# Optimization experiments

Hardware: AMD Instinct MI355X
Metric: run time of the kernel (lower is better)

## Reference

```python
import jax, jax.numpy as jnp
import numpy as np

H, B, T, C = 1024, 256, 256, 10

def setup_inputs() -> dict:
    key = jax.random.key(0)
    ks = jax.random.split(key, 10)
    def xav(k, shape):
        fan_in, fan_out = shape[1], shape[0]
        lim = jnp.sqrt(6.0 / (fan_in + fan_out))
        return jax.random.uniform(k, shape, jnp.float32, -lim, lim)
    return {
        "x": jax.random.normal(ks[0], (B, T), jnp.float32),
        "W_gx": xav(ks[1], (H, 1)), "W_gh": xav(ks[2], (H, H)),
        "W_ix": xav(ks[3], (H, 1)), "W_ih": xav(ks[4], (H, H)),
        "W_fx": xav(ks[5], (H, 1)), "W_fh": xav(ks[6], (H, H)),
        "W_ox": xav(ks[7], (H, 1)), "W_oh": xav(ks[8], (H, H)),
        "W_ph": xav(ks[9], (C, H)),
        "b_g": jnp.zeros((B,), jnp.float32), "b_i": jnp.zeros((B,), jnp.float32),
        "b_f": jnp.zeros((B,), jnp.float32), "b_o": jnp.zeros((B,), jnp.float32),
        "b_p": jnp.zeros((B,), jnp.float32),
    }

def reference(x, W_gx, W_gh, W_ix, W_ih, W_fx, W_fh, W_ox, W_oh, W_ph,
              b_g, b_i, b_f, b_o, b_p):
    batch = x.shape[0]
    hidden = W_gh.shape[0]
    xs = x.T  # [T, B]; per-step x_t is a [1, B] row (input_dim = 1)

    def step(carry, x_t):
        h, c = carry                       # [H, B] each
        xr = x_t[None, :]                  # [1, B]
        g = jnp.tanh(W_gx @ xr + W_gh @ h + b_g)          # [H, B] + [B] broadcasts per column
        i = jax.nn.sigmoid(W_ix @ xr + W_ih @ h + b_i)
        f = jax.nn.sigmoid(W_fx @ xr + W_fh @ h + b_f)
        o = jax.nn.sigmoid(W_ox @ xr + W_oh @ h + b_o)
        c_new = g * i + c * f
        h_new = jnp.tanh(c_new) * o
        return (h_new, c_new), None

    h0 = jnp.zeros((hidden, batch), x.dtype)
    c0 = jnp.zeros((hidden, batch), x.dtype)
    (h_T, _), _ = jax.lax.scan(step, (h0, c0), xs)
    p = W_ph @ h_T + b_p                   # [C, B]
    y = jax.nn.softmax(p, axis=1)          # faithful: softmax over dim=1 (batch axis)
    return y.T                             # [B, C]
```

## Files before the change

kernel.cpp:

```cpp
#include <hip/hip_runtime.h>
#include <hip/hip_bf16.h>


#define H 1024
#define B 256
#define T 256
#define NCLS 10

typedef __attribute__((ext_vector_type(8))) short short8;
typedef __attribute__((ext_vector_type(4))) float f32x4;

__device__ inline unsigned short bf16_bits(float f) {
    union { __hip_bfloat16 h; unsigned short u; } cv;
    cv.h = __float2bfloat16(f);
    return cv.u;
}


__global__ __launch_bounds__(512)
__attribute__((amdgpu_waves_per_eu(2, 2)))
void lstm_persist(
    const float* __restrict__ x,
    const float* __restrict__ Wgh, const float* __restrict__ Wih,
    const float* __restrict__ Wfh, const float* __restrict__ Woh,
    const float* __restrict__ Wgx, const float* __restrict__ Wix,
    const float* __restrict__ Wfx, const float* __restrict__ Wox,
    const float* __restrict__ bg, const float* __restrict__ bi,
    const float* __restrict__ bf_, const float* __restrict__ bo,
    char* __restrict__ frag,
    unsigned* __restrict__ flags,
    float* __restrict__ hfin)
{
    __shared__ __align__(16) char hstage[65536];
    __shared__ float zb[2][4][32][36];
    __shared__ float wxl[4][32];
    __shared__ float bsl[4][32];

    const int tid  = threadIdx.x;
    const int lane = tid & 63;
    const int wave = tid >> 6;
    const int gate = wave & 3;
    const int kh   = wave >> 2;
    const int bt = blockIdx.x & 7;
    const int jt = blockIdx.x >> 3;
    const int j0 = jt * 32;
    const int b0 = bt * 32;

    if (tid < 128) {
        int g = tid >> 5, r = tid & 31;
        const float* wx = (g == 0) ? Wgx : (g == 1) ? Wix : (g == 2) ? Wfx : Wox;
        const float* bb = (g == 0) ? bg  : (g == 1) ? bi  : (g == 2) ? bf_ : bo;
        wxl[g][r] = wx[j0 + r];
        bsl[g][r] = bb[b0 + r];
    }

    const float* Wh = (gate == 0) ? Wgh : (gate == 1) ? Wih : (gate == 2) ? Wfh : Woh;
    short8 awreg[2][16];
#pragma unroll
    for (int mt = 0; mt < 2; ++mt) {
        const float* wrow = Wh + (j0 + 16 * mt + (lane & 15)) * H
                          + kh * 512 + ((lane >> 4) * 8);
#pragma unroll
        for (int c = 0; c < 16; ++c) {
            const float4 f0 = *(const float4*)(wrow + c * 32);
            const float4 f1 = *(const float4*)(wrow + c * 32 + 4);
            short8 s;
            s[0] = (short)bf16_bits(f0.x); s[1] = (short)bf16_bits(f0.y);
            s[2] = (short)bf16_bits(f0.z); s[3] = (short)bf16_bits(f0.w);
            s[4] = (short)bf16_bits(f1.x); s[5] = (short)bf16_bits(f1.y);
            s[6] = (short)bf16_bits(f1.z); s[7] = (short)bf16_bits(f1.w);
            awreg[mt][c] = s;
        }
    }
#pragma unroll
    for (int mt = 0; mt < 2; ++mt)
#pragma unroll
        for (int c = 0; c < 16; ++c)
            __asm__ volatile("" : "+a"(awreg[mt][c]));

    float creg[2] = {0.f, 0.f};
    const int nn = tid & 31;
    const int aa = tid >> 5;

    unsigned* myflag = &flags[blockIdx.x * 32];
    unsigned* pollflag = &flags[(((unsigned)lane & 31) * 8 + bt) * 32];

    for (int t = 0; t < T; ++t) {
        const float xv = x[(b0 + nn) * T + t];

        if (wave == 0) {
            const unsigned target = (unsigned)t;
            while (true) {
                unsigned v = __hip_atomic_load(pollflag, __ATOMIC_RELAXED,
                                               __HIP_MEMORY_SCOPE_AGENT);
                if (__all((int)(v >= target))) break;
                __builtin_amdgcn_s_sleep(1);
            }
        }
        __syncthreads();

        {
            const char* gbase = frag + (t & 1) * 524288 + bt * 65536 + tid * 16;
            short8 v0, v1, v2, v3, v4, v5, v6, v7;
            __asm__ volatile(
                "global_load_dwordx4 %0, %8, off sc0 sc1\n\t"
                "global_load_dwordx4 %1, %9, off sc0 sc1\n\t"
                "global_load_dwordx4 %2, %10, off sc0 sc1\n\t"
                "global_load_dwordx4 %3, %11, off sc0 sc1\n\t"
                "global_load_dwordx4 %4, %12, off sc0 sc1\n\t"
                "global_load_dwordx4 %5, %13, off sc0 sc1\n\t"
                "global_load_dwordx4 %6, %14, off sc0 sc1\n\t"
                "global_load_dwordx4 %7, %15, off sc0 sc1\n\t"
                "s_waitcnt vmcnt(0)"
                : "=&v"(v0), "=&v"(v1), "=&v"(v2), "=&v"(v3),
                  "=&v"(v4), "=&v"(v5), "=&v"(v6), "=&v"(v7)
                : "v"(gbase),         "v"(gbase + 8192),
                  "v"(gbase + 16384), "v"(gbase + 24576),
                  "v"(gbase + 32768), "v"(gbase + 40960),
                  "v"(gbase + 49152), "v"(gbase + 57344)
                : "memory");
            short8* dd = (short8*)hstage;
            dd[tid +    0] = v0;  dd[tid +  512] = v1;
            dd[tid + 1024] = v2;  dd[tid + 1536] = v3;
            dd[tid + 2048] = v4;  dd[tid + 2560] = v5;
            dd[tid + 3072] = v6;  dd[tid + 3584] = v7;
        }
        __syncthreads();

        f32x4 a00 = {0.f,0.f,0.f,0.f}, a01 = a00, a10 = a00, a11 = a00;
#pragma unroll
        for (int c = 0; c < 16; ++c) {
            const int cg = kh * 16 + c;
            short8 bf0 = *(const short8*)(hstage + cg * 1024 + lane * 16);
            short8 bf1 = *(const short8*)(hstage + 32768 + cg * 1024 + lane * 16);
            a00 = __builtin_amdgcn_mfma_f32_16x16x32_bf16(awreg[0][c], bf0, a00, 0, 0, 0);
            a01 = __builtin_amdgcn_mfma_f32_16x16x32_bf16(awreg[0][c], bf1, a01, 0, 0, 0);
            a10 = __builtin_amdgcn_mfma_f32_16x16x32_bf16(awreg[1][c], bf0, a10, 0, 0, 0);
            a11 = __builtin_amdgcn_mfma_f32_16x16x32_bf16(awreg[1][c], bf1, a11, 0, 0, 0);
        }

        {
            const int cn = lane & 15;
            const int rb = (lane >> 4) * 4;
#pragma unroll
            for (int r = 0; r < 4; ++r) {
                zb[kh][gate][ 0 + rb + r][ 0 + cn] = a00[r];
                zb[kh][gate][ 0 + rb + r][16 + cn] = a01[r];
                zb[kh][gate][16 + rb + r][ 0 + cn] = a10[r];
                zb[kh][gate][16 + rb + r][16 + cn] = a11[r];
            }
        }
        __syncthreads();

        unsigned short hb[2];
#pragma unroll
        for (int q = 0; q < 2; ++q) {
            const int jl = 2 * aa + q;
            float zg = (zb[0][0][jl][nn] + zb[1][0][jl][nn]) + wxl[0][jl] * xv + bsl[0][nn];
            float zi = (zb[0][1][jl][nn] + zb[1][1][jl][nn]) + wxl[1][jl] * xv + bsl[1][nn];
            float zf = (zb[0][2][jl][nn] + zb[1][2][jl][nn]) + wxl[2][jl] * xv + bsl[2][nn];
            float zo = (zb[0][3][jl][nn] + zb[1][3][jl][nn]) + wxl[3][jl] * xv + bsl[3][nn];
            float g  = tanhf(zg);
            float ig = 1.f / (1.f + expf(-zi));
            float fg = 1.f / (1.f + expf(-zf));
            float og = 1.f / (1.f + expf(-zo));
            creg[q] = g * ig + creg[q] * fg;
            float hn = tanhf(creg[q]) * og;
            hb[q] = bf16_bits(hn);
            if (t == T - 1) hfin[(j0 + jl) * B + (b0 + nn)] = hn;
        }
        {
            const unsigned val = (unsigned)hb[0] | ((unsigned)hb[1] << 16);
            short* fb = (short*)(frag + ((t + 1) & 1) * 524288);
            short* fdst = fb + ((2 * bt + (nn >> 4)) * 32 + jt) * 512
                        + ((aa >> 2) * 16 + (nn & 15)) * 8 + (aa & 3) * 2;
            __hip_atomic_store((unsigned*)fdst, val, __ATOMIC_RELAXED,
                               __HIP_MEMORY_SCOPE_AGENT);
        }

        __syncthreads();
        if (tid == 0) {
            __asm__ volatile("s_waitcnt vmcnt(0)" ::: "memory");
            __hip_atomic_store(myflag, (unsigned)(t + 1), __ATOMIC_RELAXED,
                               __HIP_MEMORY_SCOPE_AGENT);
        }
    }
}

__global__ __launch_bounds__(256) void lstm_final(
    const float* __restrict__ Wph, const float* __restrict__ hfin,
    const float* __restrict__ bp, float* __restrict__ out)
{
    __shared__ float sh[256];
    __shared__ float shm, shs;
    int c = blockIdx.x;
    int b = threadIdx.x;
    float acc = bp[b];
    const float* wr = Wph + c * H;
    for (int k = 0; k < H; ++k)
        acc += wr[k] * hfin[k * B + b];

    sh[b] = acc;
    __syncthreads();
    for (int s = 128; s > 0; s >>= 1) {
        if (b < s) sh[b] = fmaxf(sh[b], sh[b + s]);
        __syncthreads();
    }
    if (b == 0) shm = sh[0];
    __syncthreads();
    float e = expf(acc - shm);
    sh[b] = e;
    __syncthreads();
    for (int s = 128; s > 0; s >>= 1) {
        if (b < s) sh[b] += sh[b + s];
        __syncthreads();
    }
    if (b == 0) shs = sh[0];
    __syncthreads();
    out[b * NCLS + c] = e / shs;
}

extern "C" void kernel_launch(void* const* d_in, const int* in_sizes, int n_in,
                              void* d_out, int out_size, void* d_ws, size_t ws_size,
                              hipStream_t stream)
{
    const float* x   = (const float*)d_in[0];
    const float* Wgx = (const float*)d_in[1];
    const float* Wgh = (const float*)d_in[2];
    const float* Wix = (const float*)d_in[3];
    const float* Wih = (const float*)d_in[4];
    const float* Wfx = (const float*)d_in[5];
    const float* Wfh = (const float*)d_in[6];
    const float* Wox = (const float*)d_in[7];
    const float* Woh = (const float*)d_in[8];
    const float* Wph = (const float*)d_in[9];
    const float* bg  = (const float*)d_in[10];
    const float* bi  = (const float*)d_in[11];
    const float* bfv = (const float*)d_in[12];
    const float* bo  = (const float*)d_in[13];
    const float* bp  = (const float*)d_in[14];

    char* ws = (char*)d_ws;
    char* frag = ws;
    unsigned* flags = (unsigned*)(ws + 1048576);
    float* hfin = (float*)(ws + 1081344);

    hipMemsetAsync(frag, 0, 524288, stream);
    hipMemsetAsync(flags, 0, 32768, stream);

    lstm_persist<<<256, 512, 0, stream>>>(
        x, Wgh, Wih, Wfh, Woh, Wgx, Wix, Wfx, Wox,
        bg, bi, bfv, bo, frag, flags, hfin);

    lstm_final<<<NCLS, 256, 0, stream>>>(Wph, hfin, bp, (float*)d_out);
}
```

Measured before the change: 1.216 ms.

## Detect same-XCC batch groups, relax cache bypass, skip step-zero matmul, fast activations

Each block reads its XCC id and publishes it. Blocks sharing a batch tile then check whether all of them sit on one XCC; if so, the h exchange drops the sc1 bit on loads and uses plain volatile stores, avoiding the L2-bypassing path. The t=0 recurrent matmul and the frag memset are skipped because h0 is zero. tanh and sigmoid switch to exp2/rcp intrinsics. The risks are lower activation accuracy and reliance on L2 coherence within one XCC, which the code assumes but does not enforce.

```diff
diff --git a/kernel.cpp b/kernel.cpp
--- a/kernel.cpp
+++ b/kernel.cpp
@@ -14,6 +14,16 @@
     union { __hip_bfloat16 h; unsigned short u; } cv;
     cv.h = __float2bfloat16(f);
     return cv.u;
+}
+
+#define L2E 1.4426950408889634f
+__device__ inline float sigm_fast(float x) {
+    float e = __builtin_amdgcn_exp2f(-L2E * x);
+    return __builtin_amdgcn_rcpf(1.0f + e);
+}
+__device__ inline float tanh_fast(float x) {
+    float e = __builtin_amdgcn_exp2f((2.0f * L2E) * x);
+    return 1.0f - 2.0f * __builtin_amdgcn_rcpf(1.0f + e);
 }
 
 
@@ -29,12 +39,14 @@
     const float* __restrict__ bf_, const float* __restrict__ bo,
     char* __restrict__ frag,
     unsigned* __restrict__ flags,
+    unsigned* __restrict__ det,
     float* __restrict__ hfin)
 {
     __shared__ __align__(16) char hstage[65536];
     __shared__ float zb[2][4][32][36];
     __shared__ float wxl[4][32];
     __shared__ float bsl[4][32];
+    __shared__ int sh_lcl;
 
     const int tid  = threadIdx.x;
     const int lane = tid & 63;
@@ -46,6 +58,13 @@
     const int j0 = jt * 32;
     const int b0 = bt * 32;
 
+    unsigned xcc;
+    __asm__ volatile("s_getreg_b32 %0, hwreg(HW_REG_XCC_ID)" : "=s"(xcc));
+    xcc &= 7u;
+    if (tid == 0)
+        __hip_atomic_store(&det[bt * 32 + jt], xcc + 1u,
+                           __ATOMIC_RELAXED, __HIP_MEMORY_SCOPE_AGENT);
+
     if (tid < 128) {
         int g = tid >> 5, r = tid & 31;
         const float* wx = (g == 0) ? Wgx : (g == 1) ? Wix : (g == 2) ? Wfx : Wox;
@@ -78,6 +97,20 @@
         for (int c = 0; c < 16; ++c)
             __asm__ volatile("" : "+a"(awreg[mt][c]));
 
+    if (wave == 0) {
+        unsigned v;
+        while (true) {
+            v = __hip_atomic_load(&det[bt * 32 + (lane & 31)],
+                                  __ATOMIC_RELAXED, __HIP_MEMORY_SCOPE_AGENT);
+            if (__all((int)(v != 0u))) break;
+            __builtin_amdgcn_s_sleep(1);
+        }
+        int same = __all((int)(v == xcc + 1u));
+        if (tid == 0) sh_lcl = same;
+    }
+    __syncthreads();
+    const bool lcl = (sh_lcl != 0);
+
     float creg[2] = {0.f, 0.f};
     const int nn = tid & 31;
     const int aa = tid >> 5;
@@ -99,44 +132,67 @@
         }
         __syncthreads();
 
-        {
-            const char* gbase = frag + (t & 1) * 524288 + bt * 65536 + tid * 16;
-            short8 v0, v1, v2, v3, v4, v5, v6, v7;
-            __asm__ volatile(
-                "global_load_dwordx4 %0, %8, off sc0 sc1\n\t"
-                "global_load_dwordx4 %1, %9, off sc0 sc1\n\t"
-                "global_load_dwordx4 %2, %10, off sc0 sc1\n\t"
-                "global_load_dwordx4 %3, %11, off sc0 sc1\n\t"
-                "global_load_dwordx4 %4, %12, off sc0 sc1\n\t"
-                "global_load_dwordx4 %5, %13, off sc0 sc1\n\t"
-                "global_load_dwordx4 %6, %14, off sc0 sc1\n\t"
-                "global_load_dwordx4 %7, %15, off sc0 sc1\n\t"
-                "s_waitcnt vmcnt(0)"
-                : "=&v"(v0), "=&v"(v1), "=&v"(v2), "=&v"(v3),
-                  "=&v"(v4), "=&v"(v5), "=&v"(v6), "=&v"(v7)
-                : "v"(gbase),         "v"(gbase + 8192),
-                  "v"(gbase + 16384), "v"(gbase + 24576),
-                  "v"(gbase + 32768), "v"(gbase + 40960),
-                  "v"(gbase + 49152), "v"(gbase + 57344)
-                : "memory");
-            short8* dd = (short8*)hstage;
-            dd[tid +    0] = v0;  dd[tid +  512] = v1;
-            dd[tid + 1024] = v2;  dd[tid + 1536] = v3;
-            dd[tid + 2048] = v4;  dd[tid + 2560] = v5;
-            dd[tid + 3072] = v6;  dd[tid + 3584] = v7;
-        }
-        __syncthreads();
-
         f32x4 a00 = {0.f,0.f,0.f,0.f}, a01 = a00, a10 = a00, a11 = a00;
-#pragma unroll
-        for (int c = 0; c < 16; ++c) {
-            const int cg = kh * 16 + c;
-            short8 bf0 = *(const short8*)(hstage + cg * 1024 + lane * 16);
-            short8 bf1 = *(const short8*)(hstage + 32768 + cg * 1024 + lane * 16);
-            a00 = __builtin_amdgcn_mfma_f32_16x16x32_bf16(awreg[0][c], bf0, a00, 0, 0, 0);
-            a01 = __builtin_amdgcn_mfma_f32_16x16x32_bf16(awreg[0][c], bf1, a01, 0, 0, 0);
-            a10 = __builtin_amdgcn_mfma_f32_16x16x32_bf16(awreg[1][c], bf0, a10, 0, 0, 0);
-            a11 = __builtin_amdgcn_mfma_f32_16x16x32_bf16(awreg[1][c], bf1, a11, 0, 0, 0);
+
+        if (t > 0) {
+            {
+                const char* gbase = frag + (t & 1) * 524288 + bt * 65536 + tid * 16;
+                short8 v0, v1, v2, v3, v4, v5, v6, v7;
+                if (lcl) {
+                    __asm__ volatile(
+                        "global_load_dwordx4 %0, %8, off sc0\n\t"
+                        "global_load_dwordx4 %1, %9, off sc0\n\t"
+                        "global_load_dwordx4 %2, %10, off sc0\n\t"
+                        "global_load_dwordx4 %3, %11, off sc0\n\t"
+                        "global_load_dwordx4 %4, %12, off sc0\n\t"
+                        "global_load_dwordx4 %5, %13, off sc0\n\t"
+                        "global_load_dwordx4 %6, %14, off sc0\n\t"
+                        "global_load_dwordx4 %7, %15, off sc0\n\t"
+                        "s_waitcnt vmcnt(0)"
+                        : "=&v"(v0), "=&v"(v1), "=&v"(v2), "=&v"(v3),
+                          "=&v"(v4), "=&v"(v5), "=&v"(v6), "=&v"(v7)
+                        : "v"(gbase),         "v"(gbase + 8192),
+                          "v"(gbase + 16384), "v"(gbase + 24576),
+                          "v"(gbase + 32768), "v"(gbase + 40960),
+                          "v"(gbase + 49152), "v"(gbase + 57344)
+                        : "memory");
+                } else {
+                    __asm__ volatile(
+                        "global_load_dwordx4 %0, %8, off sc0 sc1\n\t"
+                        "global_load_dwordx4 %1, %9, off sc0 sc1\n\t"
+                        "global_load_dwordx4 %2, %10, off sc0 sc1\n\t"
+                        "global_load_dwordx4 %3, %11, off sc0 sc1\n\t"
+                        "global_load_dwordx4 %4, %12, off sc0 sc1\n\t"
+                        "global_load_dwordx4 %5, %13, off sc0 sc1\n\t"
+                        "global_load_dwordx4 %6, %14, off sc0 sc1\n\t"
+                        "global_load_dwordx4 %7, %15, off sc0 sc1\n\t"
+                        "s_waitcnt vmcnt(0)"
+                        : "=&v"(v0), "=&v"(v1), "=&v"(v2), "=&v"(v3),
+                          "=&v"(v4), "=&v"(v5), "=&v"(v6), "=&v"(v7)
+                        : "v"(gbase),         "v"(gbase + 8192),
+                          "v"(gbase + 16384), "v"(gbase + 24576),
+                          "v"(gbase + 32768), "v"(gbase + 40960),
+                          "v"(gbase + 49152), "v"(gbase + 57344)
+                        : "memory");
+                }
+                short8* dd = (short8*)hstage;
+                dd[tid +    0] = v0;  dd[tid +  512] = v1;
+                dd[tid + 1024] = v2;  dd[tid + 1536] = v3;
+                dd[tid + 2048] = v4;  dd[tid + 2560] = v5;
+                dd[tid + 3072] = v6;  dd[tid + 3584] = v7;
+            }
+            __syncthreads();
+
+#pragma unroll
+            for (int c = 0; c < 16; ++c) {
+                const int cg = kh * 16 + c;
+                short8 bf0 = *(const short8*)(hstage + cg * 1024 + lane * 16);
+                short8 bf1 = *(const short8*)(hstage + 32768 + cg * 1024 + lane * 16);
+                a00 = __builtin_amdgcn_mfma_f32_16x16x32_bf16(awreg[0][c], bf0, a00, 0, 0, 0);
+                a01 = __builtin_amdgcn_mfma_f32_16x16x32_bf16(awreg[0][c], bf1, a01, 0, 0, 0);
+                a10 = __builtin_amdgcn_mfma_f32_16x16x32_bf16(awreg[1][c], bf0, a10, 0, 0, 0);
+                a11 = __builtin_amdgcn_mfma_f32_16x16x32_bf16(awreg[1][c], bf1, a11, 0, 0, 0);
+            }
         }
 
         {
@@ -160,12 +216,12 @@
             float zi = (zb[0][1][jl][nn] + zb[1][1][jl][nn]) + wxl[1][jl] * xv + bsl[1][nn];
             float zf = (zb[0][2][jl][nn] + zb[1][2][jl][nn]) + wxl[2][jl] * xv + bsl[2][nn];
             float zo = (zb[0][3][jl][nn] + zb[1][3][jl][nn]) + wxl[3][jl] * xv + bsl[3][nn];
-            float g  = tanhf(zg);
-            float ig = 1.f / (1.f + expf(-zi));
-            float fg = 1.f / (1.f + expf(-zf));
-            float og = 1.f / (1.f + expf(-zo));
+            float g  = tanh_fast(zg);
+            float ig = sigm_fast(zi);
+            float fg = sigm_fast(zf);
+            float og = sigm_fast(zo);
             creg[q] = g * ig + creg[q] * fg;
-            float hn = tanhf(creg[q]) * og;
+            float hn = tanh_fast(creg[q]) * og;
             hb[q] = bf16_bits(hn);
             if (t == T - 1) hfin[(j0 + jl) * B + (b0 + nn)] = hn;
         }
@@ -174,8 +230,12 @@
             short* fb = (short*)(frag + ((t + 1) & 1) * 524288);
             short* fdst = fb + ((2 * bt + (nn >> 4)) * 32 + jt) * 512
                         + ((aa >> 2) * 16 + (nn & 15)) * 8 + (aa & 3) * 2;
-            __hip_atomic_store((unsigned*)fdst, val, __ATOMIC_RELAXED,
-                               __HIP_MEMORY_SCOPE_AGENT);
+            if (lcl) {
+                *(volatile unsigned*)fdst = val;
+            } else {
+                __hip_atomic_store((unsigned*)fdst, val, __ATOMIC_RELAXED,
+                                   __HIP_MEMORY_SCOPE_AGENT);
+            }
         }
 
         __syncthreads();
@@ -243,14 +303,14 @@
     char* ws = (char*)d_ws;
     char* frag = ws;
     unsigned* flags = (unsigned*)(ws + 1048576);
-    float* hfin = (float*)(ws + 1081344);
-
-    hipMemsetAsync(frag, 0, 524288, stream);
-    hipMemsetAsync(flags, 0, 32768, stream);
+    unsigned* det   = (unsigned*)(ws + 1081344);
+    float* hfin = (float*)(ws + 1085440);
+
+    hipMemsetAsync(flags, 0, 36864, stream);
 
     lstm_persist<<<256, 512, 0, stream>>>(
         x, Wgh, Wih, Wfh, Woh, Wgx, Wix, Wfx, Wox,
-        bg, bi, bfv, bo, frag, flags, hfin);
+        bg, bi, bfv, bo, frag, flags, det, hfin);
 
     lstm_final<<<NCLS, 256, 0, stream>>>(Wph, hfin, bp, (float*)d_out);
 }
```

Result: faster. 1.160 ms (-4.6%).
